# Kernel optimization log

Hardware: AMD Instinct MI355X
Metric: run time of the kernel (lower is better)

## Reference

```python
import jax, jax.numpy as jnp
import numpy as np

STRIDE = 2
PADDING = 1


def setup_inputs() -> dict:
    key = jax.random.key(0)
    k1, k2, k3, k4, k5 = jax.random.split(key, 5)
    B, C, H, W = 32, 128, 64, 64
    O, kh, kw = 256, 3, 3
    ah = H + 2 * PADDING - (kh - 1)  # 64
    oh = ah // STRIDE                # 32 (divisible -> ceil == floor, rest == 0)
    inputs = {
        "input": jax.random.normal(k1, (B, C, H, W), dtype=jnp.float32),
        "weight": jax.random.normal(k2, (O, C, kh, kw), dtype=jnp.float32) * 0.05,
        "bias": jax.random.normal(k3, (O,), dtype=jnp.float32) * 0.05,
        "selh": jax.random.randint(k4, (oh, oh), 0, STRIDE, dtype=jnp.int32),
        "selw": jax.random.randint(k5, (oh, oh), 0, STRIDE, dtype=jnp.int32),
    }
    return inputs


def reference(input, weight, bias, selh, selw):
    # Faithful to SConv2dAvg.forward with stoch=True, mask == -1, stride=2:
    # unfold(input, k, pad, stride=1) -> stochastic gather of one position per
    # stride x stride cell (offsets selh/selw) -> GEMM with flattened weight -> reshape.
    B, C, H, W = input.shape
    O, _, kh, kw = weight.shape
    ah = H + 2 * PADDING - (kh - 1)
    aw = W + 2 * PADDING - (kw - 1)
    oh = ah // STRIDE  # divisible by construction; ceil_mode correction is a no-op
    ow = aw // STRIDE
    xp = jnp.pad(input, ((0, 0), (0, 0), (PADDING, PADDING), (PADDING, PADDING)))
    # selected unfold positions in the afterconv grid
    rng_h = selh + (jnp.arange(oh, dtype=selh.dtype) * STRIDE)[:, None]   # [oh, ow]
    rng_w = selw + (jnp.arange(ow, dtype=selw.dtype) * STRIDE)[None, :]   # [oh, ow]
    # gather k x k patches directly (equivalent to gathering unfold columns)
    rows = rng_h[:, :, None, None] + jnp.arange(kh)[None, None, :, None]  # [oh, ow, kh, 1]
    cols = rng_w[:, :, None, None] + jnp.arange(kw)[None, None, None, :]  # [oh, ow, 1, kw]
    patches = xp[:, :, rows, cols]  # [B, C, oh, ow, kh, kw]
    out = jnp.einsum('bchwij,ocij->bohw', patches, weight) + bias[None, :, None, None]
    return out  # [B, O, oh, ow]
```

## Files before the change

### kernel.cpp

```cpp
#include <hip/hip_runtime.h>
#include <hip/hip_bf16.h>


typedef short bf16x8 __attribute__((ext_vector_type(8)));
typedef float f32x4  __attribute__((ext_vector_type(4)));

#define WPRE_BYTES (18 * 256 * 64 * 2)
#define TRANS_BYTES (32 * 66 * 66 * 128 * 2)
#define TOTAL_WS (WPRE_BYTES + TRANS_BYTES)

__device__ __forceinline__ unsigned short f2bf(float x) {
  unsigned u = __float_as_uint(x);
  return (unsigned short)((u + 0x7fffu + ((u >> 16) & 1u)) >> 16);
}
__device__ __forceinline__ unsigned pk2(float a, float b) {
  unsigned ua = __float_as_uint(a), ub = __float_as_uint(b);
  return ((ua + 0x7fffu + ((ua >> 16) & 1u)) >> 16) |
         ((ub + 0x7fffu + ((ub >> 16) & 1u)) & 0xffff0000u);
}
__device__ __forceinline__ bf16x8 ld_frag(const uint4* a) {
  union { uint4 u; bf16x8 s; } cv; cv.u = *a; return cv.s;
}
__device__ __forceinline__ void async16(const void* g, void* l) {
  __builtin_amdgcn_global_load_lds(
      (__attribute__((address_space(1))) void*)(void*)g,
      (__attribute__((address_space(3))) void*)l, 16, 0, 0);
}

__global__ __launch_bounds__(256) void prep(const float* __restrict__ in,
                                            const float* __restrict__ w,
                                            unsigned short* __restrict__ tp,
                                            unsigned short* __restrict__ wpre) {
  const int tid = threadIdx.x;
  if (blockIdx.x >= 66) {
    const int L   = ((((blockIdx.x - 66) << 5) + blockIdx.y) << 8) + tid;
    const int e   = L & 7;
    const int pos = (L >> 3) & 7;
    const int o   = (L >> 6) & 255;
    const int t   = L >> 14;
    const int c   = ((t & 1) << 6) + ((pos ^ (o & 7)) << 3) + e;
    wpre[L] = f2bf(w[(o * 128 + c) * 9 + (t >> 1)]);
    return;
  }
  __shared__ float lds[128 * 65];
  const int hp = blockIdx.x;
  const int b  = blockIdx.y;
  uint4* rowp = (uint4*)(tp + (size_t)(b * 66 + hp) * 66 * 128);
  uint4 z; z.x = z.y = z.z = z.w = 0u;
  if (hp == 0 || hp == 65) {
    for (int s = tid; s < 1056; s += 256) rowp[s] = z;
    return;
  }
  const int h = hp - 1;
  const float* src = in + ((size_t)b << 19) + (h << 6);
  const int ww4 = (tid & 15) << 2;
  const int c0  = tid >> 4;
#pragma unroll
  for (int pass = 0; pass < 8; ++pass) {
    int c = (pass << 4) + c0;
    float4 v = *(const float4*)(src + ((size_t)c << 12) + ww4);
    float* lp = lds + c * 65 + ww4;
    lp[0] = v.x; lp[1] = v.y; lp[2] = v.z; lp[3] = v.w;
  }
  __syncthreads();
  for (int s = tid; s < 1056; s += 256) {
    if (s < 16 || s >= 1040) { rowp[s] = z; continue; }
    int idx = s - 16;
    int wq = idx >> 4, c8 = idx & 15;
    const float* lp = lds + (c8 << 3) * 65 + wq;
    uint4 d;
    d.x = pk2(lp[0],   lp[65]);
    d.y = pk2(lp[130], lp[195]);
    d.z = pk2(lp[260], lp[325]);
    d.w = pk2(lp[390], lp[455]);
    rowp[s] = d;
  }
}

__global__ __launch_bounds__(512, 1) void sconv_mfma9(
    const unsigned short* __restrict__ tp,
    const unsigned short* __restrict__ wpre,
    const float* __restrict__ bias,
    const int* __restrict__ selh,
    const int* __restrict__ selw,
    float* __restrict__ out)
{
  __shared__ uint4 Alds[2][1024];
  __shared__ uint4 Blds[2][2048];
  __shared__ float bias_s[256];

  const int tid = threadIdx.x;
  const int d0  = blockIdx.x;
  const int blk = ((d0 & 7) << 5) | (d0 >> 3);
  const int b   = blk >> 3;
  const int y0  = (blk & 7) << 2;

  if (tid < 256) bias_s[tid] = bias[tid];

  const int wv = tid >> 6, ln = tid & 63;
  const int lo = ln & 15, hi = ln >> 4;

  const int p = tid >> 2;
  const int q = tid & 3;
  int asrc;
  {
    const int py = y0 + (p >> 5), px = p & 31;
    asrc = (((b * 66 + 2 * py + selh[(py << 5) | px]) * 66
             + 2 * px + selw[(py << 5) | px]) << 8);
  }
  const int cxor = q ^ (p & 3);
  const char* tbase = (const char*)tp;
  const char* wsrc = (const char*)wpre + (((wv << 8) + ln) << 4);

  const int wo = wv >> 1;
  const int wp = wv & 1;

  f32x4 acc[4][4] = {};

#define STAGE(BUF, T)                                                         \
  do {                                                                        \
    const int tap_ = (T) >> 1;                                                \
    const int di_  = (tap_ >= 6) ? 2 : ((tap_ >= 3) ? 1 : 0);                 \
    const int dj_  = tap_ - 3 * di_;                                          \
    const int ab_  = asrc + ((di_ * 66 + dj_) << 8) + (((T) & 1) << 7);       \
         \
    async16(tbase + ab_ + (cxor << 4),        &Alds[BUF][(wv << 7)]);         \
    async16(tbase + ab_ + ((4 + cxor) << 4),  &Alds[BUF][(wv << 7) + 64]);    \
                                                \
    async16(wsrc + ((T) << 15),         &Blds[BUF][(wv << 8)]);               \
    async16(wsrc + ((T) << 15) + 1024,  &Blds[BUF][(wv << 8) + 64]);          \
    async16(wsrc + ((T) << 15) + 2048,  &Blds[BUF][(wv << 8) + 128]);         \
    async16(wsrc + ((T) << 15) + 3072,  &Blds[BUF][(wv << 8) + 192]);         \
  } while (0)

#define COMPUTE(BUF)                                                          \
  do {                                                                        \
    const uint4* A_ = &Alds[BUF][0];                                          \
    const uint4* B_ = &Blds[BUF][0];                                          \
    bf16x8 FW[4][2], FP[4][2];                                                \
    _Pragma("unroll")                                                         \
    for (int f = 0; f < 4; ++f) {                                             \
      const int O = (wo << 6) + (f << 4) + lo;                                \
      const int P = (wp << 6) + (f << 4) + lo;                                \
      _Pragma("unroll")                                                       \
      for (int ks = 0; ks < 2; ++ks) {                                        \
        FW[f][ks] = ld_frag(B_ + (O << 3) + (((ks << 2) | hi) ^ (lo & 7)));   \
        FP[f][ks] = ld_frag(A_ + ((P >> 4) << 7) + (ks << 6)                  \
                            + ((P & 15) << 2) + (hi ^ (P & 3)));              \
      }                                                                       \
    }                                                                         \
    __builtin_amdgcn_s_setprio(1);                                            \
    _Pragma("unroll")                                                         \
    for (int fo = 0; fo < 4; ++fo)                                            \
      _Pragma("unroll")                                                       \
      for (int fp = 0; fp < 4; ++fp)                                          \
        _Pragma("unroll")                                                     \
        for (int ks = 0; ks < 2; ++ks)                                        \
          acc[fo][fp] = __builtin_amdgcn_mfma_f32_16x16x32_bf16(              \
              FW[fo][ks], FP[fp][ks], acc[fo][fp], 0, 0, 0);                  \
    __builtin_amdgcn_s_setprio(0);                                            \
  } while (0)

  asm volatile("s_waitcnt vmcnt(0) lgkmcnt(0)" ::: "memory");
  __builtin_amdgcn_s_barrier();
  asm volatile("" ::: "memory");

  STAGE(0, 0);

#pragma unroll
  for (int t = 0; t < 18; ++t) {
    if (t < 17) {
      STAGE((t + 1) & 1, t + 1);
      asm volatile("s_waitcnt vmcnt(6)" ::: "memory");
    } else {
      asm volatile("s_waitcnt vmcnt(0)" ::: "memory");
    }
    __builtin_amdgcn_s_barrier();
    asm volatile("" ::: "memory");
    COMPUTE(t & 1);
    asm volatile("s_waitcnt lgkmcnt(0)" ::: "memory");
    __builtin_amdgcn_s_barrier();
    asm volatile("" ::: "memory");
  }
#undef STAGE
#undef COMPUTE

  float* ob = out + ((size_t)b << 18) + (y0 << 5);
#pragma unroll
  for (int fo = 0; fo < 4; ++fo) {
    const int obase = (wo << 6) + (fo << 4) + (hi << 2);
#pragma unroll
    for (int fp = 0; fp < 4; ++fp) {
      const int P = (wp << 6) + (fp << 4) + lo;
#pragma unroll
      for (int j = 0; j < 4; ++j) {
        const int o = obase + j;
        ob[((size_t)o << 10) + P] = acc[fo][fp][j] + bias_s[o];
      }
    }
  }
}

__global__ __launch_bounds__(256) void sconv_naive(
    const float* __restrict__ in, const float* __restrict__ w,
    const float* __restrict__ bias, const int* __restrict__ selh,
    const int* __restrict__ selw, float* __restrict__ out) {
  int idx = (blockIdx.x << 8) + threadIdx.x;
  if (idx >= 32 * 256 * 32 * 32) return;
  int x = idx & 31, y = (idx >> 5) & 31, o = (idx >> 10) & 255, b = idx >> 18;
  int rh0 = 2 * y + selh[(y << 5) | x] - 1;
  int rw0 = 2 * x + selw[(y << 5) | x] - 1;
  const float* inb = in + ((size_t)b << 19);
  const float* wo_ = w + o * 1152;
  float acc = bias[o];
  for (int c = 0; c < 128; ++c)
    for (int i = 0; i < 3; ++i) {
      int rh = rh0 + i;
      if (rh < 0 || rh >= 64) continue;
      for (int j = 0; j < 3; ++j) {
        int rw = rw0 + j;
        if (rw < 0 || rw >= 64) continue;
        acc += inb[(c << 12) + (rh << 6) + rw] * wo_[c * 9 + i * 3 + j];
      }
    }
  out[idx] = acc;
}

extern "C" void kernel_launch(void* const* d_in, const int* in_sizes, int n_in,
                              void* d_out, int out_size, void* d_ws, size_t ws_size,
                              hipStream_t stream) {
  const float* in   = (const float*)d_in[0];
  const float* w    = (const float*)d_in[1];
  const float* bias = (const float*)d_in[2];
  const int*   selh = (const int*)d_in[3];
  const int*   selw = (const int*)d_in[4];
  float* out = (float*)d_out;

  if (ws_size >= (size_t)TOTAL_WS) {
    unsigned short* wpre = (unsigned short*)d_ws;
    unsigned short* tp   = (unsigned short*)((char*)d_ws + WPRE_BYTES);
    prep<<<dim3(102, 32), dim3(256), 0, stream>>>(in, w, tp, wpre);
    sconv_mfma9<<<dim3(256), dim3(512), 0, stream>>>(tp, wpre, bias, selh, selw, out);
  } else {
    sconv_naive<<<dim3(32768), dim3(256), 0, stream>>>(in, w, bias, selh, selw, out);
  }
}
```

Before: 51.58 us.

## Halve K-step to 32 channels with 36 pipeline stages and smaller LDS

The main GEMM loop now consumes 32 channels per stage instead of 64, giving 36 stages over the 9 taps. The weight prepack layout and swizzle in prep change to match. Per-stage LDS buffers are halved, fewer async loads are issued per stage, and launch bounds allow more waves per SIMD. The aim is lower LDS footprint and finer-grained pipelining, at the cost of twice as many barriers and fewer MFMAs per barrier.

```diff
diff --git a/kernel.cpp b/kernel.cpp
--- a/kernel.cpp
+++ b/kernel.cpp
@@ -5,7 +5,7 @@
 typedef short bf16x8 __attribute__((ext_vector_type(8)));
 typedef float f32x4  __attribute__((ext_vector_type(4)));
 
-#define WPRE_BYTES (18 * 256 * 64 * 2)
+#define WPRE_BYTES (36 * 256 * 32 * 2)
 #define TRANS_BYTES (32 * 66 * 66 * 128 * 2)
 #define TOTAL_WS (WPRE_BYTES + TRANS_BYTES)
 
@@ -35,11 +35,11 @@
   if (blockIdx.x >= 66) {
     const int L   = ((((blockIdx.x - 66) << 5) + blockIdx.y) << 8) + tid;
     const int e   = L & 7;
-    const int pos = (L >> 3) & 7;
-    const int o   = (L >> 6) & 255;
-    const int t   = L >> 14;
-    const int c   = ((t & 1) << 6) + ((pos ^ (o & 7)) << 3) + e;
-    wpre[L] = f2bf(w[(o * 128 + c) * 9 + (t >> 1)]);
+    const int pos = (L >> 3) & 3;
+    const int o   = (L >> 5) & 255;
+    const int s   = L >> 13;
+    const int c   = ((s & 3) << 5) + ((pos ^ (o & 3)) << 3) + e;
+    wpre[L] = f2bf(w[(o * 128 + c) * 9 + (s >> 2)]);
     return;
   }
   __shared__ float lds[128 * 65];
@@ -77,7 +77,7 @@
   }
 }
 
-__global__ __launch_bounds__(512, 1) void sconv_mfma9(
+__global__ __launch_bounds__(512, 6) void sconv_mfma10(
     const unsigned short* __restrict__ tp,
     const unsigned short* __restrict__ wpre,
     const float* __restrict__ bias,
@@ -85,8 +85,8 @@
     const int* __restrict__ selw,
     float* __restrict__ out)
 {
-  __shared__ uint4 Alds[2][1024];
-  __shared__ uint4 Blds[2][2048];
+  __shared__ uint4 Alds[2][512];
+  __shared__ uint4 Blds[2][1024];
   __shared__ float bias_s[256];
 
   const int tid = threadIdx.x;
@@ -106,11 +106,10 @@
   {
     const int py = y0 + (p >> 5), px = p & 31;
     asrc = (((b * 66 + 2 * py + selh[(py << 5) | px]) * 66
-             + 2 * px + selw[(py << 5) | px]) << 8);
-  }
-  const int cxor = q ^ (p & 3);
+             + 2 * px + selw[(py << 5) | px]) << 8) + ((q ^ (p & 3)) << 4);
+  }
   const char* tbase = (const char*)tp;
-  const char* wsrc = (const char*)wpre + (((wv << 8) + ln) << 4);
+  const char* wsrc = (const char*)wpre + (tid << 4);
 
   const int wo = wv >> 1;
   const int wp = wv & 1;
@@ -119,46 +118,37 @@
 
 #define STAGE(BUF, T)                                                         \
   do {                                                                        \
-    const int tap_ = (T) >> 1;                                                \
+    const int tap_ = (T) >> 2;                                                \
     const int di_  = (tap_ >= 6) ? 2 : ((tap_ >= 3) ? 1 : 0);                 \
     const int dj_  = tap_ - 3 * di_;                                          \
-    const int ab_  = asrc + ((di_ * 66 + dj_) << 8) + (((T) & 1) << 7);       \
-         \
-    async16(tbase + ab_ + (cxor << 4),        &Alds[BUF][(wv << 7)]);         \
-    async16(tbase + ab_ + ((4 + cxor) << 4),  &Alds[BUF][(wv << 7) + 64]);    \
-                                                \
-    async16(wsrc + ((T) << 15),         &Blds[BUF][(wv << 8)]);               \
-    async16(wsrc + ((T) << 15) + 1024,  &Blds[BUF][(wv << 8) + 64]);          \
-    async16(wsrc + ((T) << 15) + 2048,  &Blds[BUF][(wv << 8) + 128]);         \
-    async16(wsrc + ((T) << 15) + 3072,  &Blds[BUF][(wv << 8) + 192]);         \
+                     \
+    async16(tbase + asrc + ((di_ * 66 + dj_) << 8) + (((T) & 3) << 6),        \
+            &Alds[BUF][(wv << 6)]);                                           \
+                                         \
+    async16(wsrc + ((T) << 14),        &Blds[BUF][(wv << 6)]);                \
+    async16(wsrc + ((T) << 14) + 8192, &Blds[BUF][(wv << 6) + 512]);          \
   } while (0)
 
-#define COMPUTE(BUF)                                                          \
-  do {                                                                        \
-    const uint4* A_ = &Alds[BUF][0];                                          \
-    const uint4* B_ = &Blds[BUF][0];                                          \
-    bf16x8 FW[4][2], FP[4][2];                                                \
-    _Pragma("unroll")                                                         \
-    for (int f = 0; f < 4; ++f) {                                             \
-      const int O = (wo << 6) + (f << 4) + lo;                                \
-      const int P = (wp << 6) + (f << 4) + lo;                                \
-      _Pragma("unroll")                                                       \
-      for (int ks = 0; ks < 2; ++ks) {                                        \
-        FW[f][ks] = ld_frag(B_ + (O << 3) + (((ks << 2) | hi) ^ (lo & 7)));   \
-        FP[f][ks] = ld_frag(A_ + ((P >> 4) << 7) + (ks << 6)                  \
-                            + ((P & 15) << 2) + (hi ^ (P & 3)));              \
-      }                                                                       \
-    }                                                                         \
-    __builtin_amdgcn_s_setprio(1);                                            \
-    _Pragma("unroll")                                                         \
-    for (int fo = 0; fo < 4; ++fo)                                            \
-      _Pragma("unroll")                                                       \
-      for (int fp = 0; fp < 4; ++fp)                                          \
-        _Pragma("unroll")                                                     \
-        for (int ks = 0; ks < 2; ++ks)                                        \
-          acc[fo][fp] = __builtin_amdgcn_mfma_f32_16x16x32_bf16(              \
-              FW[fo][ks], FP[fp][ks], acc[fo][fp], 0, 0, 0);                  \
-    __builtin_amdgcn_s_setprio(0);                                            \
+#define COMPUTE(BUF)                                                         \
+  do {                                                                       \
+    const uint4* A_ = &Alds[BUF][0];                                         \
+    const uint4* B_ = &Blds[BUF][0];                                         \
+    bf16x8 FW[4], FP[4];                                                     \
+    _Pragma("unroll")                                                        \
+    for (int f = 0; f < 4; ++f) {                                            \
+      const int O = (wo << 6) + (f << 4) + lo;                               \
+      const int P = (wp << 6) + (f << 4) + lo;                               \
+      FW[f] = ld_frag(B_ + (O << 2) + (hi ^ (O & 3)));                       \
+      FP[f] = ld_frag(A_ + (P << 2) + (hi ^ (P & 3)));                       \
+    }                                                                        \
+    __builtin_amdgcn_s_setprio(1);                                           \
+    _Pragma("unroll")                                                        \
+    for (int fo = 0; fo < 4; ++fo)                                           \
+      _Pragma("unroll")                                                      \
+      for (int fp = 0; fp < 4; ++fp)                                         \
+        acc[fo][fp] = __builtin_amdgcn_mfma_f32_16x16x32_bf16(               \
+            FW[fo], FP[fp], acc[fo][fp], 0, 0, 0);                           \
+    __builtin_amdgcn_s_setprio(0);                                           \
   } while (0)
 
   asm volatile("s_waitcnt vmcnt(0) lgkmcnt(0)" ::: "memory");
@@ -167,14 +157,10 @@
 
   STAGE(0, 0);
 
-#pragma unroll
-  for (int t = 0; t < 18; ++t) {
-    if (t < 17) {
-      STAGE((t + 1) & 1, t + 1);
-      asm volatile("s_waitcnt vmcnt(6)" ::: "memory");
-    } else {
-      asm volatile("s_waitcnt vmcnt(0)" ::: "memory");
-    }
+#pragma unroll 4
+  for (int t = 0; t < 35; ++t) {
+    STAGE((t + 1) & 1, t + 1);
+    asm volatile("s_waitcnt vmcnt(3)" ::: "memory");
     __builtin_amdgcn_s_barrier();
     asm volatile("" ::: "memory");
     COMPUTE(t & 1);
@@ -182,6 +168,10 @@
     __builtin_amdgcn_s_barrier();
     asm volatile("" ::: "memory");
   }
+  asm volatile("s_waitcnt vmcnt(0)" ::: "memory");
+  __builtin_amdgcn_s_barrier();
+  asm volatile("" ::: "memory");
+  COMPUTE(1);
 #undef STAGE
 #undef COMPUTE
 
@@ -240,7 +230,7 @@
     unsigned short* wpre = (unsigned short*)d_ws;
     unsigned short* tp   = (unsigned short*)((char*)d_ws + WPRE_BYTES);
     prep<<<dim3(102, 32), dim3(256), 0, stream>>>(in, w, tp, wpre);
-    sconv_mfma9<<<dim3(256), dim3(512), 0, stream>>>(tp, wpre, bias, selh, selw, out);
+    sconv_mfma10<<<dim3(256), dim3(512), 0, stream>>>(tp, wpre, bias, selh, selw, out);
   } else {
     sconv_naive<<<dim3(32768), dim3(256), 0, stream>>>(in, w, bias, selh, selw, out);
   }
```

Result: slower. 162.3 us (+214.7%).
